# Kernel tuning notes

Measured on AMD Instinct MI355X. Metric: run time of the kernel, lower is better.

Reference implementation:

```python
import jax, jax.numpy as jnp
import numpy as np

B, T, I = 64, 512, 512
H, L = 512, 2


def setup_inputs() -> dict:
    key = jax.random.key(0)
    ks = jax.random.split(key, 5)
    s = 1.0 / np.sqrt(H)
    return {
        "x": jax.random.normal(ks[0], (B, T, I), dtype=jnp.float32),
        "h0": jnp.zeros((L, B, H), dtype=jnp.float32),
        "Wih": jax.random.uniform(ks[1], (L, H, I), dtype=jnp.float32, minval=-s, maxval=s),
        "bih": jax.random.uniform(ks[2], (L, H), dtype=jnp.float32, minval=-s, maxval=s),
        "Whh": jax.random.uniform(ks[3], (L, H, H), dtype=jnp.float32, minval=-s, maxval=s),
        "bhh": jax.random.uniform(ks[4], (L, H), dtype=jnp.float32, minval=-s, maxval=s),
    }


def reference(x, h0, Wih, bih, Whh, bhh):
    # x: [B, T, I] (batch_first) -> scan over time axis
    xt = jnp.swapaxes(x, 0, 1)  # [T, B, I]

    def step(hidden, x_t):
        # hidden: [L, B, H], x_t: [B, I]
        inp = x_t
        new_h = []
        for l in range(L):
            h = jnp.tanh(inp @ Wih[l].T + bih[l] + hidden[l] @ Whh[l].T + bhh[l])
            new_h.append(h)
            inp = h  # dropout=0.0 -> identity between layers
        return jnp.stack(new_h, axis=0), inp

    hidden_final, outs = jax.lax.scan(step, h0, xt)
    outputs = jnp.swapaxes(outs, 0, 1)  # [B, T, H]
    return outputs, hidden_final
```

## Files before the change

kernel.cpp:

```cpp
#include <hip/hip_runtime.h>
#include <hip/hip_fp16.h>

#define HD 512
#define Bsz 64
#define Tlen 512
#define GB 4
#define RING 16

typedef _Float16 h2v __attribute__((ext_vector_type(2)));
typedef unsigned u32x4 __attribute__((ext_vector_type(4)));
typedef unsigned long long ull;

__device__ __forceinline__ float dot2acc(unsigned a, unsigned b, float c) {
    return __builtin_amdgcn_fdot2(__builtin_bit_cast(h2v, a),
                                  __builtin_bit_cast(h2v, b), c, false);
}

__device__ __forceinline__ u32x4 mall_ld16(const void* p) {
    u32x4 r;
    asm volatile("global_load_dwordx4 %0, %1, off sc0 sc1\n\ts_waitcnt vmcnt(0)"
                 : "=v"(r) : "v"(p) : "memory");
    return r;
}
__device__ __forceinline__ void mall_st16(void* p, u32x4 v) {
    asm volatile("global_store_dwordx4 %0, %1, off sc0 sc1"
                 :: "v"(p), "v"(v) : "memory");
}
__device__ __forceinline__ unsigned mall_ld4(const unsigned* p) {
    unsigned r;
    asm volatile("global_load_dword %0, %1, off sc0 sc1\n\ts_waitcnt vmcnt(0)"
                 : "=v"(r) : "v"(p) : "memory");
    return r;
}
__device__ __forceinline__ void mall_st4(unsigned* p, unsigned v) {
    asm volatile("global_store_dword %0, %1, off sc0 sc1"
                 :: "v"(p), "v"(v) : "memory");
}

__device__ __forceinline__ bool valid8(u32x4 v) {
    unsigned bad = 0;
#pragma unroll
    for (int i = 0; i < 4; ++i) {
        bad |= ((v[i] & 0xFFFFu) == 0xFFFFu);
        bad |= ((v[i] >> 16)     == 0xFFFFu);
    }
    return bad == 0u;
}

__device__ __forceinline__ u32x4 ring_wait16(const void* p) {
    u32x4 v;
    bool ok = false;
    for (;;) {
        if (!ok) { v = mall_ld16(p); ok = valid8(v); }
        if (!__any((int)(!ok))) break;
        __builtin_amdgcn_s_sleep(1);
    }
    return v;
}

__device__ __forceinline__ void cvt4s(_Float16* d, float4 v) {
    union { ull u; _Float16 h[4]; } t;
    t.h[0] = (_Float16)v.x; t.h[1] = (_Float16)v.y;
    t.h[2] = (_Float16)v.z; t.h[3] = (_Float16)v.w;
    *(ull*)d = t.u;
}

__device__ __forceinline__ void gemm4(const u32x4* __restrict__ Ip, const u32x4* wr,
                                      int kq, int kbase, float acc[2][4]) {
#pragma unroll
    for (int i = 0; i < 4; ++i) {
        const int k8 = kbase + kq + 16 * i;
        const u32x4 w0 = wr[i * 2 + 0], w1 = wr[i * 2 + 1];
#pragma unroll
        for (int b = 0; b < 4; ++b) {
            const u32x4 h = Ip[k8 * 4 + b];
#pragma unroll
            for (int e = 0; e < 4; ++e) {
                acc[0][b] = dot2acc(w0[e], h[e], acc[0][b]);
                acc[1][b] = dot2acc(w1[e], h[e], acc[1][b]);
            }
        }
    }
}

__global__ __launch_bounds__(512, 1) void rnn_fullring(
    const float* __restrict__ x, const float* __restrict__ h0in,
    const float* __restrict__ Wih, const float* __restrict__ bih,
    const float* __restrict__ Whh, const float* __restrict__ bhh,
    _Float16* __restrict__ H0r, _Float16* __restrict__ H1r,
    float* __restrict__ out)
{
    __shared__ _Float16 inb[128 * GB * 8] __attribute__((aligned(16)));
    __shared__ float    part[256 * 17];
    __shared__ _Float16 hout[256] __attribute__((aligned(16)));

    const int bid = blockIdx.x;
    const int g   = bid & 15;
    const int sl  = bid >> 4;
    const int l   = sl >> 3;
    const int rb  = sl & 7;
    const int tid = threadIdx.x;
    const int rh = tid >> 8, kq = (tid >> 4) & 15, rq = tid & 15;

    u32x4 wreg[16];
    {
        const float* WI = Wih + (size_t)l * HD * HD;
        const float* WH = Whh + (size_t)l * HD * HD;
#pragma unroll
        for (int ph = 0; ph < 2; ++ph) {
            const float* W = ph ? WH : WI;
#pragma unroll
            for (int i = 0; i < 4; ++i)
#pragma unroll
                for (int ri = 0; ri < 2; ++ri) {
                    const int row = rb * 64 + rq + 16 * (2 * rh + ri);
                    const float* p = W + (size_t)row * HD + (kq + 16 * i) * 8;
                    union { u32x4 u; _Float16 h[8]; } v;
#pragma unroll
                    for (int e = 0; e < 8; ++e) v.h[e] = (_Float16)p[e];
                    wreg[ph * 8 + i * 2 + ri] = v.u;
                }
        }
    }

    float bias = 0.f;
    if (tid < 256) {
        const int rowg = rb * 64 + (tid & 63);
        bias = bih[l * HD + rowg] + bhh[l * HD + rowg];
    }

    _Float16* ringo = l ? H1r : H0r;
    const u32x4* Ip = (const u32x4*)inb;

    const int bb = tid >> 7;
    const int k4 = tid & 127;
    const int bglobS = g * GB + bb;

    float4 xreg;
    if (l == 0) xreg = *(const float4*)(x + (size_t)bglobS * Tlen * HD + k4 * 4);

    for (int t = 0; t < Tlen; ++t) {
        float acc[2][4] = {{0, 0, 0, 0}, {0, 0, 0, 0}};

        if (l == 0) {
            cvt4s(&inb[((k4 >> 1) * GB + bb) * 8 + (k4 & 1) * 4], xreg);
            __syncthreads();
            if (t + 1 < Tlen)
                xreg = *(const float4*)(x + ((size_t)bglobS * Tlen + t + 1) * HD + k4 * 4);
            gemm4(Ip, wreg, kq, 0, acc);
            if (t == 0) {
                if (tid < 256) {
                    int b2 = tid >> 6, k8 = tid & 63;
                    const float* src = h0in + (size_t)(g * GB + b2) * HD + k8 * 8;
                    cvt4s(&inb[((64 + k8) * GB + b2) * 8],     *(const float4*)src);
                    cvt4s(&inb[((64 + k8) * GB + b2) * 8 + 4], *(const float4*)(src + 4));
                }
            } else if (tid < 256) {
                int b2 = tid >> 6, k8 = tid & 63;
                u32x4 v = ring_wait16(H0r + ((size_t)(t - 1) * Bsz + g * GB + b2) * HD + k8 * 8);
                *(u32x4*)&inb[((64 + k8) * GB + b2) * 8] = v;
            }
            __syncthreads();
            gemm4(Ip, wreg + 8, kq, 64, acc);
        } else {
            if (tid < 256) {
                int b2 = tid >> 6, k8 = tid & 63;
                u32x4 v = ring_wait16(H0r + ((size_t)t * Bsz + g * GB + b2) * HD + k8 * 8);
                *(u32x4*)&inb[(k8 * GB + b2) * 8] = v;
            } else if (t == 0) {
                int t2 = tid - 256; int b2 = t2 >> 6, k8 = t2 & 63;
                const float* src = h0in + (size_t)(Bsz + g * GB + b2) * HD + k8 * 8;
                cvt4s(&inb[((64 + k8) * GB + b2) * 8],     *(const float4*)src);
                cvt4s(&inb[((64 + k8) * GB + b2) * 8 + 4], *(const float4*)(src + 4));
            } else {
                int t2 = tid - 256; int b2 = t2 >> 6, k8 = t2 & 63;
                u32x4 v = ring_wait16(H1r + ((size_t)(t - 1) * Bsz + g * GB + b2) * HD + k8 * 8);
                *(u32x4*)&inb[((64 + k8) * GB + b2) * 8] = v;
            }
            __syncthreads();
            gemm4(Ip, wreg, kq, 0, acc);
            gemm4(Ip, wreg + 8, kq, 64, acc);
        }

#pragma unroll
        for (int ri = 0; ri < 2; ++ri)
#pragma unroll
            for (int b = 0; b < 4; ++b)
                part[(size_t)(b * 64 + rq + 16 * (2 * rh + ri)) * 17 + kq] = acc[ri][b];
        __syncthreads();
        if (tid < 256) {
            float s = bias;
#pragma unroll
            for (int k2 = 0; k2 < 16; ++k2) s += part[(size_t)tid * 17 + k2];
            const float hv = tanhf(s);
            hout[tid] = (_Float16)hv;
            const int rowg = rb * 64 + (tid & 63);
            const int bo = g * GB + (tid >> 6);
            if (l == 1) out[((size_t)bo * Tlen + t) * HD + rowg] = hv;
            if (t == Tlen - 1)
                out[(size_t)Bsz * Tlen * HD + ((size_t)l * Bsz + bo) * HD + rowg] = hv;
        }
        __syncthreads();

        if (tid < 32) {
            u32x4 v = *(const u32x4*)&hout[(tid >> 3) * 64 + (tid & 7) * 8];
            mall_st16(ringo + ((size_t)t * Bsz + g * GB + (tid >> 3)) * HD + rb * 64 + (tid & 7) * 8, v);
        }
    }
}

__device__ __forceinline__ void poll2(unsigned* a, unsigned* b) {
    const int ln = threadIdx.x;
    unsigned* fp = nullptr;
    if (ln < 8)       { if (a) fp = a + ln; }
    else if (ln < 16) { if (b) fp = b + (ln - 8); }
    for (;;) {
        unsigned v = fp ? mall_ld4(fp) : 1u;
        if (!__any((int)(v != 1u))) break;
        __builtin_amdgcn_s_sleep(1);
    }
}

__global__ __launch_bounds__(512, 1) void rnn_chain(
    const float* __restrict__ x, const float* __restrict__ h0in,
    const float* __restrict__ Wih, const float* __restrict__ bih,
    const float* __restrict__ Whh, const float* __restrict__ bhh,
    _Float16* __restrict__ H0r, _Float16* __restrict__ H1r,
    unsigned* f0, unsigned* f1, float* __restrict__ out)
{
    __shared__ _Float16 inb[128 * GB * 8] __attribute__((aligned(16)));
    __shared__ float    part[256 * 17];
    __shared__ _Float16 hout[256] __attribute__((aligned(16)));

    const int bid = blockIdx.x;
    const int g   = bid & 15;
    const int sl  = bid >> 4;
    const int l   = sl >> 3;
    const int rb  = sl & 7;
    const int tid = threadIdx.x;
    const int rh = tid >> 8, kq = (tid >> 4) & 15, rq = tid & 15;

    u32x4 wreg[16];
    {
        const float* WI = Wih + (size_t)l * HD * HD;
        const float* WH = Whh + (size_t)l * HD * HD;
#pragma unroll
        for (int ph = 0; ph < 2; ++ph) {
            const float* W = ph ? WH : WI;
#pragma unroll
            for (int i = 0; i < 4; ++i)
#pragma unroll
                for (int ri = 0; ri < 2; ++ri) {
                    const int row = rb * 64 + rq + 16 * (2 * rh + ri);
                    const float* p = W + (size_t)row * HD + (kq + 16 * i) * 8;
                    union { u32x4 u; _Float16 h[8]; } v;
#pragma unroll
                    for (int e = 0; e < 8; ++e) v.h[e] = (_Float16)p[e];
                    wreg[ph * 8 + i * 2 + ri] = v.u;
                }
        }
    }

    float bias = 0.f;
    if (tid < 256) {
        const int rowg = rb * 64 + (tid & 63);
        bias = bih[l * HD + rowg] + bhh[l * HD + rowg];
    }

    unsigned* fown = (l ? f1 : f0) + ((size_t)g * Tlen) * 8 + rb;
    _Float16* ringo = l ? H1r : H0r;
    const u32x4* Ip = (const u32x4*)inb;

    const int bb = tid >> 7;
    const int k4 = tid & 127;
    const int bglobS = g * GB + bb;

    float4 xreg;
    if (l == 0) xreg = *(const float4*)(x + (size_t)bglobS * Tlen * HD + k4 * 4);

    for (int t = 0; t < Tlen; ++t) {
        const int slot = t & (RING - 1);
        float acc[2][4] = {{0, 0, 0, 0}, {0, 0, 0, 0}};

        if (l == 0) {
            cvt4s(&inb[((k4 >> 1) * GB + bb) * 8 + (k4 & 1) * 4], xreg);
            __syncthreads();
            if (t + 1 < Tlen)
                xreg = *(const float4*)(x + ((size_t)bglobS * Tlen + t + 1) * HD + k4 * 4);
            gemm4(Ip, wreg, kq, 0, acc);
            if (tid < 64)
                poll2((t > 0)     ? f0 + ((size_t)g * Tlen + (t - 1)) * 8 : nullptr,
                      (t >= RING) ? f1 + ((size_t)g * Tlen + (t - RING)) * 8 : nullptr);
            __syncthreads();
            if (t == 0) {
                if (tid < 256) {
                    int b2 = tid >> 6, k8 = tid & 63;
                    const float* src = h0in + (size_t)(g * GB + b2) * HD + k8 * 8;
                    cvt4s(&inb[((64 + k8) * GB + b2) * 8],     *(const float4*)src);
                    cvt4s(&inb[((64 + k8) * GB + b2) * 8 + 4], *(const float4*)(src + 4));
                }
            } else if (tid < 256) {
                int b2 = tid >> 6, k8 = tid & 63;
                u32x4 v = mall_ld16(H0r + ((size_t)((t - 1) & (RING - 1)) * Bsz + g * GB + b2) * HD + k8 * 8);
                *(u32x4*)&inb[((64 + k8) * GB + b2) * 8] = v;
            }
            __syncthreads();
            gemm4(Ip, wreg + 8, kq, 64, acc);
        } else {
            if (tid < 64)
                poll2(f0 + ((size_t)g * Tlen + t) * 8,
                      (t > 0) ? f1 + ((size_t)g * Tlen + (t - 1)) * 8 : nullptr);
            __syncthreads();
            if (tid < 256) {
                int b2 = tid >> 6, k8 = tid & 63;
                u32x4 v = mall_ld16(H0r + ((size_t)slot * Bsz + g * GB + b2) * HD + k8 * 8);
                *(u32x4*)&inb[(k8 * GB + b2) * 8] = v;
            } else if (t == 0) {
                int t2 = tid - 256; int b2 = t2 >> 6, k8 = t2 & 63;
                const float* src = h0in + (size_t)(Bsz + g * GB + b2) * HD + k8 * 8;
                cvt4s(&inb[((64 + k8) * GB + b2) * 8],     *(const float4*)src);
                cvt4s(&inb[((64 + k8) * GB + b2) * 8 + 4], *(const float4*)(src + 4));
            } else {
                int t2 = tid - 256; int b2 = t2 >> 6, k8 = t2 & 63;
                u32x4 v = mall_ld16(H1r + ((size_t)((t - 1) & (RING - 1)) * Bsz + g * GB + b2) * HD + k8 * 8);
                *(u32x4*)&inb[((64 + k8) * GB + b2) * 8] = v;
            }
            __syncthreads();
            gemm4(Ip, wreg, kq, 0, acc);
            gemm4(Ip, wreg + 8, kq, 64, acc);
        }

#pragma unroll
        for (int ri = 0; ri < 2; ++ri)
#pragma unroll
            for (int b = 0; b < 4; ++b)
                part[(size_t)(b * 64 + rq + 16 * (2 * rh + ri)) * 17 + kq] = acc[ri][b];
        __syncthreads();
        if (tid < 256) {
            float s = bias;
#pragma unroll
            for (int k2 = 0; k2 < 16; ++k2) s += part[(size_t)tid * 17 + k2];
            const float hv = tanhf(s);
            hout[tid] = (_Float16)hv;
            const int rowg = rb * 64 + (tid & 63);
            const int bo = g * GB + (tid >> 6);
            if (l == 1) out[((size_t)bo * Tlen + t) * HD + rowg] = hv;
            if (t == Tlen - 1)
                out[(size_t)Bsz * Tlen * HD + ((size_t)l * Bsz + bo) * HD + rowg] = hv;
        }
        __syncthreads();

        if (tid < 32) {
            u32x4 v = *(const u32x4*)&hout[(tid >> 3) * 64 + (tid & 7) * 8];
            mall_st16(ringo + ((size_t)slot * Bsz + g * GB + (tid >> 3)) * HD + rb * 64 + (tid & 7) * 8, v);
        }
        if (tid < 64) {
            asm volatile("s_waitcnt vmcnt(0)" ::: "memory");
            if (tid == 0) mall_st4(fown + (size_t)t * 8, 1u);
        }
    }
}

extern "C" void kernel_launch(void* const* d_in, const int* in_sizes, int n_in,
                              void* d_out, int out_size, void* d_ws, size_t ws_size,
                              hipStream_t stream) {
    const float* x   = (const float*)d_in[0];
    const float* h0  = (const float*)d_in[1];
    const float* Wih = (const float*)d_in[2];
    const float* bih = (const float*)d_in[3];
    const float* Whh = (const float*)d_in[4];
    const float* bhh = (const float*)d_in[5];
    float* out = (float*)d_out;
    char* ws = (char*)d_ws;

    const size_t ring_bytes = (size_t)Tlen * Bsz * HD * sizeof(_Float16);

    if (ws_size >= 2 * ring_bytes) {
        _Float16* H0r = (_Float16*)ws;
        _Float16* H1r = (_Float16*)(ws + ring_bytes);
        (void)hipMemsetAsync(ws, 0xFF, 2 * ring_bytes, stream);
        void* args[] = { (void*)&x, (void*)&h0, (void*)&Wih, (void*)&bih,
                         (void*)&Whh, (void*)&bhh, (void*)&H0r, (void*)&H1r,
                         (void*)&out };
        (void)hipLaunchCooperativeKernel((const void*)rnn_fullring, dim3(256),
                                         dim3(512), args, 0, stream);
    } else {
        unsigned* f0  = (unsigned*)ws;
        unsigned* f1  = (unsigned*)(ws + (256u << 10));
        _Float16* H0r = (_Float16*)(ws + (512u << 10));
        _Float16* H1r = (_Float16*)(ws + (512u << 10) + (1u << 20));
        (void)hipMemsetAsync(ws, 0, 512u << 10, stream);
        void* args[] = { (void*)&x, (void*)&h0, (void*)&Wih, (void*)&bih,
                         (void*)&Whh, (void*)&bhh, (void*)&H0r, (void*)&H1r,
                         (void*)&f0, (void*)&f1, (void*)&out };
        (void)hipLaunchCooperativeKernel((const void*)rnn_chain, dim3(256),
                                         dim3(512), args, 0, stream);
    }
}
```

Baseline: 1.413 ms.

## Issue recurrent-state ring loads early and overlap with input GEMM; batch-major LDS layout

```diff
diff --git a/kernel.cpp b/kernel.cpp
--- a/kernel.cpp
+++ b/kernel.cpp
@@ -37,6 +37,14 @@
                  :: "v"(p), "v"(v) : "memory");
 }
 
+__device__ __forceinline__ void probe_ld16(u32x4* d, const void* p) {
+    asm volatile("global_load_dwordx4 %0, %1, off sc0 sc1"
+                 : "=v"(*d) : "v"(p) : "memory");
+}
+__device__ __forceinline__ void probe_wait(u32x4* d) {
+    asm volatile("s_waitcnt vmcnt(0)" : "+v"(*d) :: "memory");
+}
+
 __device__ __forceinline__ bool valid8(u32x4 v) {
     unsigned bad = 0;
 #pragma unroll
@@ -45,6 +53,16 @@
         bad |= ((v[i] >> 16)     == 0xFFFFu);
     }
     return bad == 0u;
+}
+
+__device__ __forceinline__ u32x4 probe_finish(u32x4 v, const void* p) {
+    bool ok = valid8(v);
+    for (;;) {
+        if (!__any((int)(!ok))) break;
+        __builtin_amdgcn_s_sleep(1);
+        if (!ok) { v = mall_ld16(p); ok = valid8(v); }
+    }
+    return v;
 }
 
 __device__ __forceinline__ u32x4 ring_wait16(const void* p) {
@@ -73,7 +91,7 @@
         const u32x4 w0 = wr[i * 2 + 0], w1 = wr[i * 2 + 1];
 #pragma unroll
         for (int b = 0; b < 4; ++b) {
-            const u32x4 h = Ip[k8 * 4 + b];
+            const u32x4 h = Ip[b * 128 + k8];
 #pragma unroll
             for (int e = 0; e < 4; ++e) {
                 acc[0][b] = dot2acc(w0[e], h[e], acc[0][b]);
@@ -90,7 +108,7 @@
     _Float16* __restrict__ H0r, _Float16* __restrict__ H1r,
     float* __restrict__ out)
 {
-    __shared__ _Float16 inb[128 * GB * 8] __attribute__((aligned(16)));
+    __shared__ _Float16 inb[GB * 128 * 8] __attribute__((aligned(16)));
     __shared__ float    part[256 * 17];
     __shared__ _Float16 hout[256] __attribute__((aligned(16)));
 
@@ -135,6 +153,8 @@
     const int bb = tid >> 7;
     const int k4 = tid & 127;
     const int bglobS = g * GB + bb;
+    const int b2 = (tid >> 6) & 3;
+    const int k8 = tid & 63;
 
     float4 xreg;
     if (l == 0) xreg = *(const float4*)(x + (size_t)bglobS * Tlen * HD + k4 * 4);
@@ -143,42 +163,52 @@
         float acc[2][4] = {{0, 0, 0, 0}, {0, 0, 0, 0}};
 
         if (l == 0) {
-            cvt4s(&inb[((k4 >> 1) * GB + bb) * 8 + (k4 & 1) * 4], xreg);
-            __syncthreads();
+            cvt4s(&inb[(bb * 128 + (k4 >> 1)) * 8 + (k4 & 1) * 4], xreg);
+            __syncthreads();
+            const _Float16* hp = H0r + ((size_t)(t - 1) * Bsz + g * GB + b2) * HD + k8 * 8;
+            u32x4 pv;
+            if (t == 0) {
+                if (tid < 256) {
+                    const float* src = h0in + (size_t)(g * GB + b2) * HD + k8 * 8;
+                    cvt4s(&inb[(b2 * 128 + 64 + k8) * 8],     *(const float4*)src);
+                    cvt4s(&inb[(b2 * 128 + 64 + k8) * 8 + 4], *(const float4*)(src + 4));
+                }
+            } else if (tid < 256) {
+                probe_ld16(&pv, hp);
+            }
             if (t + 1 < Tlen)
                 xreg = *(const float4*)(x + ((size_t)bglobS * Tlen + t + 1) * HD + k4 * 4);
             gemm4(Ip, wreg, kq, 0, acc);
-            if (t == 0) {
-                if (tid < 256) {
-                    int b2 = tid >> 6, k8 = tid & 63;
-                    const float* src = h0in + (size_t)(g * GB + b2) * HD + k8 * 8;
-                    cvt4s(&inb[((64 + k8) * GB + b2) * 8],     *(const float4*)src);
-                    cvt4s(&inb[((64 + k8) * GB + b2) * 8 + 4], *(const float4*)(src + 4));
-                }
-            } else if (tid < 256) {
-                int b2 = tid >> 6, k8 = tid & 63;
-                u32x4 v = ring_wait16(H0r + ((size_t)(t - 1) * Bsz + g * GB + b2) * HD + k8 * 8);
-                *(u32x4*)&inb[((64 + k8) * GB + b2) * 8] = v;
+            if (t > 0 && tid < 256) {
+                probe_wait(&pv);
+                u32x4 v = probe_finish(pv, hp);
+                *(u32x4*)&inb[(b2 * 128 + 64 + k8) * 8] = v;
             }
             __syncthreads();
             gemm4(Ip, wreg + 8, kq, 64, acc);
         } else {
-            if (tid < 256) {
-                int b2 = tid >> 6, k8 = tid & 63;
+            const _Float16* hp1 = H1r + ((size_t)(t - 1) * Bsz + g * GB + b2) * HD + k8 * 8;
+            u32x4 pv;
+            if (tid >= 256) {
+                if (t == 0) {
+                    const float* src = h0in + (size_t)(Bsz + g * GB + b2) * HD + k8 * 8;
+                    cvt4s(&inb[(b2 * 128 + 64 + k8) * 8],     *(const float4*)src);
+                    cvt4s(&inb[(b2 * 128 + 64 + k8) * 8 + 4], *(const float4*)(src + 4));
+                } else {
+                    probe_ld16(&pv, hp1);
+                }
+            } else {
                 u32x4 v = ring_wait16(H0r + ((size_t)t * Bsz + g * GB + b2) * HD + k8 * 8);
-                *(u32x4*)&inb[(k8 * GB + b2) * 8] = v;
-            } else if (t == 0) {
-                int t2 = tid - 256; int b2 = t2 >> 6, k8 = t2 & 63;
-                const float* src = h0in + (size_t)(Bsz + g * GB + b2) * HD + k8 * 8;
-                cvt4s(&inb[((64 + k8) * GB + b2) * 8],     *(const float4*)src);
-                cvt4s(&inb[((64 + k8) * GB + b2) * 8 + 4], *(const float4*)(src + 4));
-            } else {
-                int t2 = tid - 256; int b2 = t2 >> 6, k8 = t2 & 63;
-                u32x4 v = ring_wait16(H1r + ((size_t)(t - 1) * Bsz + g * GB + b2) * HD + k8 * 8);
-                *(u32x4*)&inb[((64 + k8) * GB + b2) * 8] = v;
+                *(u32x4*)&inb[(b2 * 128 + k8) * 8] = v;
             }
             __syncthreads();
             gemm4(Ip, wreg, kq, 0, acc);
+            if (t > 0 && tid >= 256) {
+                probe_wait(&pv);
+                u32x4 v = probe_finish(pv, hp1);
+                *(u32x4*)&inb[(b2 * 128 + 64 + k8) * 8] = v;
+            }
+            __syncthreads();
             gemm4(Ip, wreg + 8, kq, 64, acc);
         }
 
@@ -228,7 +258,7 @@
     _Float16* __restrict__ H0r, _Float16* __restrict__ H1r,
     unsigned* f0, unsigned* f1, float* __restrict__ out)
 {
-    __shared__ _Float16 inb[128 * GB * 8] __attribute__((aligned(16)));
+    __shared__ _Float16 inb[GB * 128 * 8] __attribute__((aligned(16)));
     __shared__ float    part[256 * 17];
     __shared__ _Float16 hout[256] __attribute__((aligned(16)));
 
@@ -283,7 +313,7 @@
         float acc[2][4] = {{0, 0, 0, 0}, {0, 0, 0, 0}};
 
         if (l == 0) {
-            cvt4s(&inb[((k4 >> 1) * GB + bb) * 8 + (k4 & 1) * 4], xreg);
+            cvt4s(&inb[(bb * 128 + (k4 >> 1)) * 8 + (k4 & 1) * 4], xreg);
             __syncthreads();
             if (t + 1 < Tlen)
                 xreg = *(const float4*)(x + ((size_t)bglobS * Tlen + t + 1) * HD + k4 * 4);
@@ -294,15 +324,15 @@
             __syncthreads();
             if (t == 0) {
                 if (tid < 256) {
-                    int b2 = tid >> 6, k8 = tid & 63;
-                    const float* src = h0in + (size_t)(g * GB + b2) * HD + k8 * 8;
-                    cvt4s(&inb[((64 + k8) * GB + b2) * 8],     *(const float4*)src);
-                    cvt4s(&inb[((64 + k8) * GB + b2) * 8 + 4], *(const float4*)(src + 4));
+                    int c2 = tid >> 6, c8 = tid & 63;
+                    const float* src = h0in + (size_t)(g * GB + c2) * HD + c8 * 8;
+                    cvt4s(&inb[(c2 * 128 + 64 + c8) * 8],     *(const float4*)src);
+                    cvt4s(&inb[(c2 * 128 + 64 + c8) * 8 + 4], *(const float4*)(src + 4));
                 }
             } else if (tid < 256) {
-                int b2 = tid >> 6, k8 = tid & 63;
-                u32x4 v = mall_ld16(H0r + ((size_t)((t - 1) & (RING - 1)) * Bsz + g * GB + b2) * HD + k8 * 8);
-                *(u32x4*)&inb[((64 + k8) * GB + b2) * 8] = v;
+                int c2 = tid >> 6, c8 = tid & 63;
+                u32x4 v = mall_ld16(H0r + ((size_t)((t - 1) & (RING - 1)) * Bsz + g * GB + c2) * HD + c8 * 8);
+                *(u32x4*)&inb[(c2 * 128 + 64 + c8) * 8] = v;
             }
             __syncthreads();
             gemm4(Ip, wreg + 8, kq, 64, acc);
@@ -312,18 +342,18 @@
                       (t > 0) ? f1 + ((size_t)g * Tlen + (t - 1)) * 8 : nullptr);
             __syncthreads();
             if (tid < 256) {
-                int b2 = tid >> 6, k8 = tid & 63;
-                u32x4 v = mall_ld16(H0r + ((size_t)slot * Bsz + g * GB + b2) * HD + k8 * 8);
-                *(u32x4*)&inb[(k8 * GB + b2) * 8] = v;
+                int c2 = tid >> 6, c8 = tid & 63;
+                u32x4 v = mall_ld16(H0r + ((size_t)slot * Bsz + g * GB + c2) * HD + c8 * 8);
+                *(u32x4*)&inb[(c2 * 128 + c8) * 8] = v;
             } else if (t == 0) {
-                int t2 = tid - 256; int b2 = t2 >> 6, k8 = t2 & 63;
-                const float* src = h0in + (size_t)(Bsz + g * GB + b2) * HD + k8 * 8;
-                cvt4s(&inb[((64 + k8) * GB + b2) * 8],     *(const float4*)src);
-                cvt4s(&inb[((64 + k8) * GB + b2) * 8 + 4], *(const float4*)(src + 4));
+                int t2 = tid - 256; int c2 = t2 >> 6, c8 = t2 & 63;
+                const float* src = h0in + (size_t)(Bsz + g * GB + c2) * HD + c8 * 8;
+                cvt4s(&inb[(c2 * 128 + 64 + c8) * 8],     *(const float4*)src);
+                cvt4s(&inb[(c2 * 128 + 64 + c8) * 8 + 4], *(const float4*)(src + 4));
             } else {
-                int t2 = tid - 256; int b2 = t2 >> 6, k8 = t2 & 63;
-                u32x4 v = mall_ld16(H1r + ((size_t)((t - 1) & (RING - 1)) * Bsz + g * GB + b2) * HD + k8 * 8);
-                *(u32x4*)&inb[((64 + k8) * GB + b2) * 8] = v;
+                int t2 = tid - 256; int c2 = t2 >> 6, c8 = t2 & 63;
+                u32x4 v = mall_ld16(H1r + ((size_t)((t - 1) & (RING - 1)) * Bsz + g * GB + c2) * HD + c8 * 8);
+                *(u32x4*)&inb[(c2 * 128 + 64 + c8) * 8] = v;
             }
             __syncthreads();
             gemm4(Ip, wreg, kq, 0, acc);
```

After: 1.451 ms. 2.7% more time.
